# Kernel optimization log

Measured on AMD Instinct MI355X. Metric: run time of the kernel, lower is better.

The kernel has to match this reference:

```python
import jax, jax.numpy as jnp
import numpy as np

B, S, D = 2, 4096, 1024
EPS = 1e-05


def setup_inputs() -> dict:
    key = jax.random.key(0)
    ks = jax.random.split(key, 7)
    x = jax.random.normal(ks[0], (B, S, D), dtype=jnp.float32)
    gamma = jnp.ones((D,), dtype=jnp.float32)
    wq, wk, wv, wa, wg, wo = (jax.random.normal(k, (D, D), dtype=jnp.float32) for k in ks[1:7])
    return {"x": x, "gamma": gamma, "wq": wq, "wk": wk, "wv": wv, "wa": wa, "wg": wg, "wo": wo}


def _rmsnorm(x, gamma):
    # original uses sum of squares (not mean) with scale = sqrt(dim)
    ss = jnp.sum(jnp.square(x), axis=-1, keepdims=True)
    inv = jax.lax.rsqrt(ss + EPS)
    return inv * x * gamma * (x.shape[-1] ** 0.5)


def _gate_loop_operator(kv, q, a):
    def binop(e_i, e_j):
        a_i, kv_i = e_i
        a_j, kv_j = e_j
        return (a_j * a_i, a_j * kv_i + kv_j)
    _, y = jax.lax.associative_scan(binop, (a, kv), axis=1)
    return q * y


def reference(x, gamma, wq, wk, wv, wa, wg, wo):
    x = _rmsnorm(x, gamma)
    q = x @ wq
    k = x @ wk
    v = x @ wv
    a = jax.nn.sigmoid(x @ wa)
    g = x @ wg
    kv = k * v
    y = _gate_loop_operator(kv, q, a)
    y = y * jax.nn.silu(g)
    return y @ wo
```

## Files before the change

kernel.cpp:

```cpp
#include <hip/hip_runtime.h>
#include <hip/hip_bf16.h>
#include <cstdint>
#include <cstddef>


typedef __bf16 bf16x8 __attribute__((ext_vector_type(8)));
typedef float f32x4 __attribute__((ext_vector_type(4)));

__device__ __forceinline__ void gload_lds16(const void* g, void* l) {
  __builtin_amdgcn_global_load_lds(
      (const __attribute__((address_space(1))) void*)g,
      (__attribute__((address_space(3))) void*)l,
      16, 0, 0);
}

__global__ __launch_bounds__(256) void wconv_k(
    const float* __restrict__ wq, const float* __restrict__ wk,
    const float* __restrict__ wv, const float* __restrict__ wa,
    const float* __restrict__ wg, const float* __restrict__ wo,
    __hip_bfloat16* __restrict__ wcatT, __hip_bfloat16* __restrict__ woT) {
  __shared__ float t[32][33];
  const float* src;
  __hip_bfloat16* dst;
  switch (blockIdx.z) {
    case 0: src = wq; dst = wcatT; break;
    case 1: src = wk; dst = wcatT + (size_t)1024 * 1024; break;
    case 2: src = wv; dst = wcatT + (size_t)2048 * 1024; break;
    case 3: src = wg; dst = wcatT + (size_t)3072 * 1024; break;
    case 4: src = wa; dst = wcatT + (size_t)4096 * 1024; break;
    default: src = wo; dst = woT; break;
  }
  const int n0 = blockIdx.x * 32;
  const int k0 = blockIdx.y * 32;
  const int tx = threadIdx.x, ty = threadIdx.y;
#pragma unroll
  for (int i = 0; i < 32; i += 8)
    t[ty + i][tx] = src[(size_t)(k0 + ty + i) * 1024 + n0 + tx];
  __syncthreads();
#pragma unroll
  for (int i = 0; i < 32; i += 8)
    dst[(size_t)(n0 + ty + i) * 1024 + k0 + tx] = __float2bfloat16(t[tx][ty + i]);
}

__global__ __launch_bounds__(256) void rmsnorm_k(
    const float* __restrict__ x, const float* __restrict__ gamma,
    __hip_bfloat16* __restrict__ xn) {
  const int row = blockIdx.x;
  const int tid = threadIdx.x;
  const float4 xv = ((const float4*)(x + (size_t)row * 1024))[tid];
  float ss = xv.x * xv.x + xv.y * xv.y + xv.z * xv.z + xv.w * xv.w;
#pragma unroll
  for (int off = 32; off >= 1; off >>= 1) ss += __shfl_xor(ss, off, 64);
  __shared__ float wss[4];
  if ((tid & 63) == 0) wss[tid >> 6] = ss;
  __syncthreads();
  const float total = wss[0] + wss[1] + wss[2] + wss[3];
  const float scale = rsqrtf(total + 1e-5f) * 32.0f;
  const float4 gv = ((const float4*)gamma)[tid];
  union { __hip_bfloat16 h[4]; ushort4 u; } ob;
  ob.h[0] = __float2bfloat16(xv.x * gv.x * scale);
  ob.h[1] = __float2bfloat16(xv.y * gv.y * scale);
  ob.h[2] = __float2bfloat16(xv.z * gv.z * scale);
  ob.h[3] = __float2bfloat16(xv.w * gv.w * scale);
  ((ushort4*)(xn + (size_t)row * 1024))[tid] = ob.u;
}

__global__ __launch_bounds__(512) void gemm256(
    const __hip_bfloat16* __restrict__ A, const __hip_bfloat16* __restrict__ Bt,
    int M, int N, int K,
    __hip_bfloat16* __restrict__ outb, int ldb, int nbcols,
    float* __restrict__ outf, int ldf) {
  __shared__ __align__(16) unsigned short As[4 * 8192];
  __shared__ __align__(16) unsigned short Bs[4 * 8192];

  const int tid = threadIdx.x;
  const int nwg = gridDim.x * gridDim.y;
  const int bid = blockIdx.y * gridDim.x + blockIdx.x;
  const int swz = (bid & 7) * (nwg >> 3) + (bid >> 3);
  const int brow = (swz / gridDim.x) * 256;
  const int bcol = (swz % gridDim.x) * 256;

  const unsigned short* Ag = (const unsigned short*)A + (size_t)brow * K;
  const unsigned short* Bg = (const unsigned short*)Bt + (size_t)bcol * K;

  const int srow = tid >> 2;
  const int sch8 = (((tid & 3) ^ ((srow >> 1) & 3)) << 3);

  auto stageA = [&](int sl) {
    unsigned short* dst = As + ((sl & 3) << 13);
    const int k0 = sl << 5;
    gload_lds16(Ag + (size_t)srow * K + k0 + sch8, dst + tid * 8);
    gload_lds16(Ag + (size_t)(srow + 128) * K + k0 + sch8, dst + 4096 + tid * 8);
  };
  auto stageB = [&](int sl) {
    unsigned short* dst = Bs + ((sl & 3) << 13);
    const int k0 = sl << 5;
    gload_lds16(Bg + (size_t)srow * K + k0 + sch8, dst + tid * 8);
    gload_lds16(Bg + (size_t)(srow + 128) * K + k0 + sch8, dst + 4096 + tid * 8);
  };

  const int lane = tid & 63;
  const int wid = tid >> 6;
  const int wr = wid >> 2;
  const int wc = wid & 3;
  const int l16 = lane & 15;
  const int k8 = lane >> 4;

  int aoff[8], boff[4];
#pragma unroll
  for (int m = 0; m < 8; ++m) {
    const int r = wr * 128 + m * 16 + l16;
    aoff[m] = r * 32 + ((k8 ^ ((r >> 1) & 3)) << 3);
  }
#pragma unroll
  for (int n = 0; n < 4; ++n) {
    const int r = wc * 64 + n * 16 + l16;
    boff[n] = r * 32 + ((k8 ^ ((r >> 1) & 3)) << 3);
  }

  f32x4 acc[8][4];
#pragma unroll
  for (int m = 0; m < 8; ++m)
#pragma unroll
    for (int n = 0; n < 4; ++n) acc[m][n] = (f32x4){0.f, 0.f, 0.f, 0.f};

  const int NS = K >> 5;
  stageA(0); stageB(0);
  stageA(1); stageB(1);
  stageA(2); stageB(2);
  asm volatile("s_waitcnt vmcnt(8)" ::: "memory");
  __builtin_amdgcn_s_barrier();

  for (int s = 0; s < NS; ++s) {
    const unsigned short* As_s = As + ((s & 3) << 13);
    const unsigned short* Bs_s = Bs + ((s & 3) << 13);
    bf16x8 af[8], bfr[4];
#pragma unroll
    for (int n = 0; n < 4; ++n) bfr[n] = *(const bf16x8*)(Bs_s + boff[n]);
#pragma unroll
    for (int m = 0; m < 4; ++m) af[m] = *(const bf16x8*)(As_s + aoff[m]);
    if (s + 3 < NS) stageA(s + 3);
#pragma unroll
    for (int m = 4; m < 8; ++m) af[m] = *(const bf16x8*)(As_s + aoff[m]);
    if (s + 3 < NS) stageB(s + 3);
    __builtin_amdgcn_s_setprio(1);
#pragma unroll
    for (int m = 0; m < 8; ++m)
#pragma unroll
      for (int n = 0; n < 4; ++n)
        acc[m][n] = __builtin_amdgcn_mfma_f32_16x16x32_bf16(af[m], bfr[n], acc[m][n], 0, 0, 0);
    __builtin_amdgcn_s_setprio(0);
    if (s < NS - 3)       asm volatile("s_waitcnt vmcnt(8)" ::: "memory");
    else if (s == NS - 3) asm volatile("s_waitcnt vmcnt(4)" ::: "memory");
    else if (s == NS - 2) asm volatile("s_waitcnt vmcnt(0)" ::: "memory");
    __builtin_amdgcn_s_barrier();
  }

  const int mb = brow + wr * 128 + k8 * 4;
  const int nb = bcol + wc * 64 + l16;
#pragma unroll
  for (int m = 0; m < 8; ++m) {
#pragma unroll
    for (int n = 0; n < 4; ++n) {
      const int col = nb + n * 16;
#pragma unroll
      for (int r = 0; r < 4; ++r) {
        const int row = mb + m * 16 + r;
        const float v = acc[m][n][r];
        if (col < nbcols) {
          outb[(size_t)row * ldb + col] = __float2bfloat16(v);
        } else {
          outf[(size_t)row * ldf + (col - nbcols)] = v;
        }
      }
    }
  }
}

__global__ __launch_bounds__(512) void gemm_n128(
    const __hip_bfloat16* __restrict__ A, const __hip_bfloat16* __restrict__ Bt,
    int M, int N, int K, float* __restrict__ outf, int ldf) {
  __shared__ __align__(16) unsigned short As[4 * 8192];
  __shared__ __align__(16) unsigned short Bs[4 * 4096];

  const int tid = threadIdx.x;
  const int nwg = gridDim.x * gridDim.y;
  const int bid = blockIdx.y * gridDim.x + blockIdx.x;
  const int swz = (bid & 7) * (nwg >> 3) + (bid >> 3);
  const int brow = (swz / gridDim.x) * 256;
  const int bcol = (swz % gridDim.x) * 128;

  const unsigned short* Ag = (const unsigned short*)A + (size_t)brow * K;
  const unsigned short* Bg = (const unsigned short*)Bt + (size_t)bcol * K;

  const int srow = tid >> 2;
  const int sch8 = (((tid & 3) ^ ((srow >> 1) & 3)) << 3);

  auto stageA = [&](int sl) {
    unsigned short* dst = As + ((sl & 3) << 13);
    const int k0 = sl << 5;
    gload_lds16(Ag + (size_t)srow * K + k0 + sch8, dst + tid * 8);
    gload_lds16(Ag + (size_t)(srow + 128) * K + k0 + sch8, dst + 4096 + tid * 8);
  };
  auto stageB = [&](int sl) {
    unsigned short* dst = Bs + ((sl & 3) << 12);
    const int k0 = sl << 5;
    gload_lds16(Bg + (size_t)srow * K + k0 + sch8, dst + tid * 8);
  };

  const int lane = tid & 63;
  const int wid = tid >> 6;
  const int wr = wid >> 2;
  const int wc = wid & 3;
  const int l16 = lane & 15;
  const int k8 = lane >> 4;

  int aoff[8], boff[2];
#pragma unroll
  for (int m = 0; m < 8; ++m) {
    const int r = wr * 128 + m * 16 + l16;
    aoff[m] = r * 32 + ((k8 ^ ((r >> 1) & 3)) << 3);
  }
#pragma unroll
  for (int n = 0; n < 2; ++n) {
    const int r = wc * 32 + n * 16 + l16;
    boff[n] = r * 32 + ((k8 ^ ((r >> 1) & 3)) << 3);
  }

  f32x4 acc[8][2];
#pragma unroll
  for (int m = 0; m < 8; ++m)
#pragma unroll
    for (int n = 0; n < 2; ++n) acc[m][n] = (f32x4){0.f, 0.f, 0.f, 0.f};

  const int NS = K >> 5;
  stageA(0); stageB(0);
  stageA(1); stageB(1);
  stageA(2); stageB(2);
  asm volatile("s_waitcnt vmcnt(6)" ::: "memory");
  __builtin_amdgcn_s_barrier();

  for (int s = 0; s < NS; ++s) {
    const unsigned short* As_s = As + ((s & 3) << 13);
    const unsigned short* Bs_s = Bs + ((s & 3) << 12);
    bf16x8 af[8], bfr[2];
    bfr[0] = *(const bf16x8*)(Bs_s + boff[0]);
    bfr[1] = *(const bf16x8*)(Bs_s + boff[1]);
#pragma unroll
    for (int m = 0; m < 4; ++m) af[m] = *(const bf16x8*)(As_s + aoff[m]);
    if (s + 3 < NS) stageA(s + 3);
#pragma unroll
    for (int m = 4; m < 8; ++m) af[m] = *(const bf16x8*)(As_s + aoff[m]);
    if (s + 3 < NS) stageB(s + 3);
    __builtin_amdgcn_s_setprio(1);
#pragma unroll
    for (int m = 0; m < 8; ++m)
#pragma unroll
      for (int n = 0; n < 2; ++n)
        acc[m][n] = __builtin_amdgcn_mfma_f32_16x16x32_bf16(af[m], bfr[n], acc[m][n], 0, 0, 0);
    __builtin_amdgcn_s_setprio(0);
    if (s < NS - 3)       asm volatile("s_waitcnt vmcnt(6)" ::: "memory");
    else if (s == NS - 3) asm volatile("s_waitcnt vmcnt(3)" ::: "memory");
    else if (s == NS - 2) asm volatile("s_waitcnt vmcnt(0)" ::: "memory");
    __builtin_amdgcn_s_barrier();
  }

  const int mb = brow + wr * 128 + k8 * 4;
  const int nb = bcol + wc * 32 + l16;
#pragma unroll
  for (int m = 0; m < 8; ++m) {
#pragma unroll
    for (int n = 0; n < 2; ++n) {
      const int col = nb + n * 16;
#pragma unroll
      for (int r = 0; r < 4; ++r) {
        const int row = mb + m * 16 + r;
        outf[(size_t)row * ldf + col] = acc[m][n][r];
      }
    }
  }
}

__global__ __launch_bounds__(256) void scan_pass1(
    const __hip_bfloat16* __restrict__ qkvg, const float* __restrict__ apre,
    float* __restrict__ Asum, float* __restrict__ Ysum) {
  const int bc = blockIdx.x;
  const int d = blockIdx.y * 256 + threadIdx.x;
  const size_t rowbase = (size_t)(bc >> 5) * 4096 + (size_t)(bc & 31) * 128;
  float y = 0.f, Ap = 1.f;
  for (int s = 0; s < 128; ++s) {
    const size_t r = rowbase + s;
    const float kk = __bfloat162float(qkvg[r * 4096 + 1024 + d]);
    const float vv = __bfloat162float(qkvg[r * 4096 + 2048 + d]);
    const float ap = apre[r * 1024 + d];
    const float a = 1.f / (1.f + __expf(-ap));
    y = fmaf(a, y, kk * vv);
    Ap *= a;
  }
  Asum[(size_t)bc * 1024 + d] = Ap;
  Ysum[(size_t)bc * 1024 + d] = y;
}

__global__ __launch_bounds__(256) void scan_pass2(
    const float* __restrict__ Asum, const float* __restrict__ Ysum,
    float* __restrict__ carry) {
  const int idx = blockIdx.x * 256 + threadIdx.x;
  const int b = idx >> 10, d = idx & 1023;
  float y = 0.f;
  for (int c = 0; c < 32; ++c) {
    const size_t o = (size_t)(b * 32 + c) * 1024 + d;
    carry[o] = y;
    y = fmaf(Asum[o], y, Ysum[o]);
  }
}

__global__ __launch_bounds__(256) void scan_pass3(
    const __hip_bfloat16* __restrict__ qkvg, const float* __restrict__ apre,
    const float* __restrict__ carry, __hip_bfloat16* __restrict__ yact) {
  const int bc = blockIdx.x;
  const int d = blockIdx.y * 256 + threadIdx.x;
  const size_t rowbase = (size_t)(bc >> 5) * 4096 + (size_t)(bc & 31) * 128;
  float y = carry[(size_t)bc * 1024 + d];
  for (int s = 0; s < 128; ++s) {
    const size_t r = rowbase + s;
    const float qq = __bfloat162float(qkvg[r * 4096 + d]);
    const float kk = __bfloat162float(qkvg[r * 4096 + 1024 + d]);
    const float vv = __bfloat162float(qkvg[r * 4096 + 2048 + d]);
    const float gg = __bfloat162float(qkvg[r * 4096 + 3072 + d]);
    const float ap = apre[r * 1024 + d];
    const float a = 1.f / (1.f + __expf(-ap));
    y = fmaf(a, y, kk * vv);
    const float sg = 1.f / (1.f + __expf(-gg));
    yact[r * 1024 + d] = __float2bfloat16(qq * y * gg * sg);
  }
}

extern "C" void kernel_launch(void* const* d_in, const int* in_sizes, int n_in,
                              void* d_out, int out_size, void* d_ws, size_t ws_size,
                              hipStream_t stream) {
  const float* x     = (const float*)d_in[0];
  const float* gamma = (const float*)d_in[1];
  const float* wq    = (const float*)d_in[2];
  const float* wk    = (const float*)d_in[3];
  const float* wv    = (const float*)d_in[4];
  const float* wa    = (const float*)d_in[5];
  const float* wg    = (const float*)d_in[6];
  const float* wo    = (const float*)d_in[7];
  float* out = (float*)d_out;

  char* ws = (char*)d_ws;
  __hip_bfloat16* wcatT = (__hip_bfloat16*)(ws);
  __hip_bfloat16* woT   = (__hip_bfloat16*)(ws + 10485760);
  __hip_bfloat16* xn    = (__hip_bfloat16*)(ws + 12582912);
  __hip_bfloat16* qkvg  = (__hip_bfloat16*)(ws + 29360128);
  float*          apre  = (float*)(ws + 96468992);
  __hip_bfloat16* yact  = (__hip_bfloat16*)(ws + 130023424);
  float*          Asum  = (float*)(ws + 146800640);
  float*          Ysum  = (float*)(ws + 147062784);
  float*          carry = (float*)(ws + 147324928);

  wconv_k<<<dim3(32, 32, 6), dim3(32, 8, 1), 0, stream>>>(wq, wk, wv, wa, wg, wo, wcatT, woT);
  rmsnorm_k<<<dim3(8192), dim3(256), 0, stream>>>(x, gamma, xn);
  gemm256<<<dim3(20, 32), dim3(512), 0, stream>>>(
      xn, wcatT, 8192, 5120, 1024, qkvg, 4096, 4096, apre, 1024);
  scan_pass1<<<dim3(64, 4), dim3(256), 0, stream>>>(qkvg, apre, Asum, Ysum);
  scan_pass2<<<dim3(8), dim3(256), 0, stream>>>(Asum, Ysum, carry);
  scan_pass3<<<dim3(64, 4), dim3(256), 0, stream>>>(qkvg, apre, carry, yact);
  gemm_n128<<<dim3(8, 32), dim3(512), 0, stream>>>(
      yact, woT, 8192, 1024, 1024, out, 1024);
}
```

Baseline: 217.7 us.

## Double-buffer B fragments in registers and interleave A loads with MFMAs

Both GEMM kernels unroll the K loop by two and keep B fragments in two register sets (even/odd), prefetching the next slice's B from LDS while the current slice's MFMAs run. A fragments are loaded progressively inside the MFMA loop, and the A and B global-to-LDS stages are merged into one call with adjusted vmcnt waits. The aim is to hide LDS read latency behind matrix-core work. The trade-off is more VGPR pressure and a more intricate barrier/wait schedule, which could cause races if the wait counts are wrong.

New measurement: 209.7 us. -3.7%, faster.

```diff
diff --git a/kernel.cpp b/kernel.cpp
--- a/kernel.cpp
+++ b/kernel.cpp
@@ -86,17 +86,14 @@
   const int srow = tid >> 2;
   const int sch8 = (((tid & 3) ^ ((srow >> 1) & 3)) << 3);
 
-  auto stageA = [&](int sl) {
-    unsigned short* dst = As + ((sl & 3) << 13);
+  auto stageAB = [&](int sl) {
+    unsigned short* dA = As + ((sl & 3) << 13);
+    unsigned short* dB = Bs + ((sl & 3) << 13);
     const int k0 = sl << 5;
-    gload_lds16(Ag + (size_t)srow * K + k0 + sch8, dst + tid * 8);
-    gload_lds16(Ag + (size_t)(srow + 128) * K + k0 + sch8, dst + 4096 + tid * 8);
-  };
-  auto stageB = [&](int sl) {
-    unsigned short* dst = Bs + ((sl & 3) << 13);
-    const int k0 = sl << 5;
-    gload_lds16(Bg + (size_t)srow * K + k0 + sch8, dst + tid * 8);
-    gload_lds16(Bg + (size_t)(srow + 128) * K + k0 + sch8, dst + 4096 + tid * 8);
+    gload_lds16(Ag + (size_t)srow * K + k0 + sch8, dA + tid * 8);
+    gload_lds16(Ag + (size_t)(srow + 128) * K + k0 + sch8, dA + 4096 + tid * 8);
+    gload_lds16(Bg + (size_t)srow * K + k0 + sch8, dB + tid * 8);
+    gload_lds16(Bg + (size_t)(srow + 128) * K + k0 + sch8, dB + 4096 + tid * 8);
   };
 
   const int lane = tid & 63;
@@ -125,35 +122,70 @@
     for (int n = 0; n < 4; ++n) acc[m][n] = (f32x4){0.f, 0.f, 0.f, 0.f};
 
   const int NS = K >> 5;
-  stageA(0); stageB(0);
-  stageA(1); stageB(1);
-  stageA(2); stageB(2);
-  asm volatile("s_waitcnt vmcnt(8)" ::: "memory");
+  stageAB(0); stageAB(1); stageAB(2);
+  asm volatile("s_waitcnt vmcnt(4)" ::: "memory");
   __builtin_amdgcn_s_barrier();
 
-  for (int s = 0; s < NS; ++s) {
-    const unsigned short* As_s = As + ((s & 3) << 13);
-    const unsigned short* Bs_s = Bs + ((s & 3) << 13);
-    bf16x8 af[8], bfr[4];
-#pragma unroll
-    for (int n = 0; n < 4; ++n) bfr[n] = *(const bf16x8*)(Bs_s + boff[n]);
-#pragma unroll
-    for (int m = 0; m < 4; ++m) af[m] = *(const bf16x8*)(As_s + aoff[m]);
-    if (s + 3 < NS) stageA(s + 3);
-#pragma unroll
-    for (int m = 4; m < 8; ++m) af[m] = *(const bf16x8*)(As_s + aoff[m]);
-    if (s + 3 < NS) stageB(s + 3);
-    __builtin_amdgcn_s_setprio(1);
-#pragma unroll
-    for (int m = 0; m < 8; ++m)
-#pragma unroll
-      for (int n = 0; n < 4; ++n)
-        acc[m][n] = __builtin_amdgcn_mfma_f32_16x16x32_bf16(af[m], bfr[n], acc[m][n], 0, 0, 0);
-    __builtin_amdgcn_s_setprio(0);
-    if (s < NS - 3)       asm volatile("s_waitcnt vmcnt(8)" ::: "memory");
-    else if (s == NS - 3) asm volatile("s_waitcnt vmcnt(4)" ::: "memory");
-    else if (s == NS - 2) asm volatile("s_waitcnt vmcnt(0)" ::: "memory");
-    __builtin_amdgcn_s_barrier();
+  bf16x8 bfE[4], bfO[4];
+  {
+    const unsigned short* B0 = Bs;
+#pragma unroll
+    for (int n = 0; n < 4; ++n) bfE[n] = *(const bf16x8*)(B0 + boff[n]);
+  }
+
+  auto slice_end = [&](int t) {
+    if (t <= NS - 4) {
+      asm volatile("s_waitcnt vmcnt(4)" ::: "memory");
+      __builtin_amdgcn_s_barrier();
+    } else if (t == NS - 3) {
+      asm volatile("s_waitcnt vmcnt(0)" ::: "memory");
+      __builtin_amdgcn_s_barrier();
+    }
+  };
+
+  for (int s = 0; s < NS; s += 2) {
+    {
+      const unsigned short* As_s = As + ((s & 3) << 13);
+      const unsigned short* Bnx = Bs + (((s + 1) & 3) << 13);
+      bf16x8 af[8];
+      af[0] = *(const bf16x8*)(As_s + aoff[0]);
+      af[1] = *(const bf16x8*)(As_s + aoff[1]);
+#pragma unroll
+      for (int n = 0; n < 4; ++n) bfO[n] = *(const bf16x8*)(Bnx + boff[n]);
+      if (s + 3 < NS) stageAB(s + 3);
+      __builtin_amdgcn_s_setprio(1);
+#pragma unroll
+      for (int m = 0; m < 8; ++m) {
+        if (m < 6) af[m + 2] = *(const bf16x8*)(As_s + aoff[m + 2]);
+#pragma unroll
+        for (int n = 0; n < 4; ++n)
+          acc[m][n] = __builtin_amdgcn_mfma_f32_16x16x32_bf16(af[m], bfE[n], acc[m][n], 0, 0, 0);
+      }
+      __builtin_amdgcn_s_setprio(0);
+      slice_end(s);
+    }
+    {
+      const unsigned short* As_s = As + (((s + 1) & 3) << 13);
+      bf16x8 af[8];
+      af[0] = *(const bf16x8*)(As_s + aoff[0]);
+      af[1] = *(const bf16x8*)(As_s + aoff[1]);
+      if (s + 2 < NS) {
+        const unsigned short* Bnx = Bs + (((s + 2) & 3) << 13);
+#pragma unroll
+        for (int n = 0; n < 4; ++n) bfE[n] = *(const bf16x8*)(Bnx + boff[n]);
+      }
+      if (s + 4 < NS) stageAB(s + 4);
+      __builtin_amdgcn_s_setprio(1);
+#pragma unroll
+      for (int m = 0; m < 8; ++m) {
+        if (m < 6) af[m + 2] = *(const bf16x8*)(As_s + aoff[m + 2]);
+#pragma unroll
+        for (int n = 0; n < 4; ++n)
+          acc[m][n] = __builtin_amdgcn_mfma_f32_16x16x32_bf16(af[m], bfO[n], acc[m][n], 0, 0, 0);
+      }
+      __builtin_amdgcn_s_setprio(0);
+      slice_end(s + 1);
+    }
   }
 
   const int mb = brow + wr * 128 + k8 * 4;
@@ -196,16 +228,13 @@
   const int srow = tid >> 2;
   const int sch8 = (((tid & 3) ^ ((srow >> 1) & 3)) << 3);
 
-  auto stageA = [&](int sl) {
-    unsigned short* dst = As + ((sl & 3) << 13);
+  auto stageAB = [&](int sl) {
+    unsigned short* dA = As + ((sl & 3) << 13);
+    unsigned short* dB = Bs + ((sl & 3) << 12);
     const int k0 = sl << 5;
-    gload_lds16(Ag + (size_t)srow * K + k0 + sch8, dst + tid * 8);
-    gload_lds16(Ag + (size_t)(srow + 128) * K + k0 + sch8, dst + 4096 + tid * 8);
-  };
-  auto stageB = [&](int sl) {
-    unsigned short* dst = Bs + ((sl & 3) << 12);
-    const int k0 = sl << 5;
-    gload_lds16(Bg + (size_t)srow * K + k0 + sch8, dst + tid * 8);
+    gload_lds16(Ag + (size_t)srow * K + k0 + sch8, dA + tid * 8);
+    gload_lds16(Ag + (size_t)(srow + 128) * K + k0 + sch8, dA + 4096 + tid * 8);
+    gload_lds16(Bg + (size_t)srow * K + k0 + sch8, dB + tid * 8);
   };
 
   const int lane = tid & 63;
@@ -234,35 +263,68 @@
     for (int n = 0; n < 2; ++n) acc[m][n] = (f32x4){0.f, 0.f, 0.f, 0.f};
 
   const int NS = K >> 5;
-  stageA(0); stageB(0);
-  stageA(1); stageB(1);
-  stageA(2); stageB(2);
-  asm volatile("s_waitcnt vmcnt(6)" ::: "memory");
+  stageAB(0); stageAB(1); stageAB(2);
+  asm volatile("s_waitcnt vmcnt(3)" ::: "memory");
   __builtin_amdgcn_s_barrier();
 
-  for (int s = 0; s < NS; ++s) {
-    const unsigned short* As_s = As + ((s & 3) << 13);
-    const unsigned short* Bs_s = Bs + ((s & 3) << 12);
-    bf16x8 af[8], bfr[2];
-    bfr[0] = *(const bf16x8*)(Bs_s + boff[0]);
-    bfr[1] = *(const bf16x8*)(Bs_s + boff[1]);
-#pragma unroll
-    for (int m = 0; m < 4; ++m) af[m] = *(const bf16x8*)(As_s + aoff[m]);
-    if (s + 3 < NS) stageA(s + 3);
-#pragma unroll
-    for (int m = 4; m < 8; ++m) af[m] = *(const bf16x8*)(As_s + aoff[m]);
-    if (s + 3 < NS) stageB(s + 3);
-    __builtin_amdgcn_s_setprio(1);
-#pragma unroll
-    for (int m = 0; m < 8; ++m)
-#pragma unroll
-      for (int n = 0; n < 2; ++n)
-        acc[m][n] = __builtin_amdgcn_mfma_f32_16x16x32_bf16(af[m], bfr[n], acc[m][n], 0, 0, 0);
-    __builtin_amdgcn_s_setprio(0);
-    if (s < NS - 3)       asm volatile("s_waitcnt vmcnt(6)" ::: "memory");
-    else if (s == NS - 3) asm volatile("s_waitcnt vmcnt(3)" ::: "memory");
-    else if (s == NS - 2) asm volatile("s_waitcnt vmcnt(0)" ::: "memory");
-    __builtin_amdgcn_s_barrier();
+  bf16x8 bfE[2], bfO[2];
+  {
+    const unsigned short* B0 = Bs;
+    bfE[0] = *(const bf16x8*)(B0 + boff[0]);
+    bfE[1] = *(const bf16x8*)(B0 + boff[1]);
+  }
+
+  auto slice_end = [&](int t) {
+    if (t <= NS - 4) {
+      asm volatile("s_waitcnt vmcnt(3)" ::: "memory");
+      __builtin_amdgcn_s_barrier();
+    } else if (t == NS - 3) {
+      asm volatile("s_waitcnt vmcnt(0)" ::: "memory");
+      __builtin_amdgcn_s_barrier();
+    }
+  };
+
+  for (int s = 0; s < NS; s += 2) {
+    {
+      const unsigned short* As_s = As + ((s & 3) << 13);
+      const unsigned short* Bnx = Bs + (((s + 1) & 3) << 12);
+      bf16x8 af[8];
+      af[0] = *(const bf16x8*)(As_s + aoff[0]);
+      af[1] = *(const bf16x8*)(As_s + aoff[1]);
+      bfO[0] = *(const bf16x8*)(Bnx + boff[0]);
+      bfO[1] = *(const bf16x8*)(Bnx + boff[1]);
+      if (s + 3 < NS) stageAB(s + 3);
+      __builtin_amdgcn_s_setprio(1);
+#pragma unroll
+      for (int m = 0; m < 8; ++m) {
+        if (m < 6) af[m + 2] = *(const bf16x8*)(As_s + aoff[m + 2]);
+        acc[m][0] = __builtin_amdgcn_mfma_f32_16x16x32_bf16(af[m], bfE[0], acc[m][0], 0, 0, 0);
+        acc[m][1] = __builtin_amdgcn_mfma_f32_16x16x32_bf16(af[m], bfE[1], acc[m][1], 0, 0, 0);
+      }
+      __builtin_amdgcn_s_setprio(0);
+      slice_end(s);
+    }
+    {
+      const unsigned short* As_s = As + (((s + 1) & 3) << 13);
+      bf16x8 af[8];
+      af[0] = *(const bf16x8*)(As_s + aoff[0]);
+      af[1] = *(const bf16x8*)(As_s + aoff[1]);
+      if (s + 2 < NS) {
+        const unsigned short* Bnx = Bs + (((s + 2) & 3) << 12);
+        bfE[0] = *(const bf16x8*)(Bnx + boff[0]);
+        bfE[1] = *(const bf16x8*)(Bnx + boff[1]);
+      }
+      if (s + 4 < NS) stageAB(s + 4);
+      __builtin_amdgcn_s_setprio(1);
+#pragma unroll
+      for (int m = 0; m < 8; ++m) {
+        if (m < 6) af[m + 2] = *(const bf16x8*)(As_s + aoff[m + 2]);
+        acc[m][0] = __builtin_amdgcn_mfma_f32_16x16x32_bf16(af[m], bfO[0], acc[m][0], 0, 0, 0);
+        acc[m][1] = __builtin_amdgcn_mfma_f32_16x16x32_bf16(af[m], bfO[1], acc[m][1], 0, 0, 0);
+      }
+      __builtin_amdgcn_s_setprio(0);
+      slice_end(s + 1);
+    }
   }
 
   const int mb = brow + wr * 128 + k8 * 4;
```
